# Performance work log

Hardware: AMD Instinct MI355X
Metric: run time of the kernel (lower is better)

Reference implementation:

```python
import jax, jax.numpy as jnp
import numpy as np

B, LQ, LK, D_WORD, D_K, D_V = 8, 2048, 2048, 1024, 128, 128
TEMPERATURE = 11.313708498984761  # sqrt(d_k)
NEG_BIG = -1e9


def setup_inputs() -> dict:
    key = jax.random.key(0)
    ks = jax.random.split(key, 7)
    scale = 1.0 / np.sqrt(D_WORD)
    return {
        "q": jax.random.normal(ks[0], (B, LQ, D_WORD), dtype=jnp.float32),
        "k": jax.random.normal(ks[1], (B, LK, D_WORD), dtype=jnp.float32),
        "v": jax.random.normal(ks[2], (B, LK, D_WORD), dtype=jnp.float32),
        "memory_lengths": jax.random.randint(ks[3], (B,), 1, LK + 1, dtype=jnp.int32),
        "Wq": jax.random.normal(ks[4], (D_WORD, D_K), dtype=jnp.float32) * scale,
        "Wk": jax.random.normal(ks[5], (D_WORD, D_K), dtype=jnp.float32) * scale,
        "Wv": jax.random.normal(ks[6], (D_WORD, D_V), dtype=jnp.float32) * scale,
    }


def reference(q, k, v, memory_lengths, Wq, Wk, Wv):
    # Projections (bias-free Dense layers)
    qs = jnp.einsum("bqw,wd->bqd", q, Wq)   # [B, LQ, D_K]
    ks = jnp.einsum("bkw,wd->bkd", k, Wk)   # [B, LK, D_K]
    vs = jnp.einsum("bkw,wd->bkd", v, Wv)   # [B, LK, D_V]
    # Scaled dot-product scores
    attn = jnp.einsum("bqd,bkd->bqk", qs, ks) / TEMPERATURE  # [B, LQ, LK]
    # Padding mask from memory_lengths (tf.sequence_mask + tile + where)
    mem_mask = jnp.arange(attn.shape[-1])[None, None, :] < memory_lengths[:, None, None]
    attn = jnp.where(mem_mask, attn, NEG_BIG)
    p = jax.nn.softmax(attn, axis=-1)
    return jnp.einsum("bqk,bkd->bqd", p, vs)  # [B, LQ, D_V]
```

## Files before the change

kernel.cpp:

```cpp
#include <hip/hip_runtime.h>

typedef _Float16 half8 __attribute__((ext_vector_type(8)));
typedef float floatx4 __attribute__((ext_vector_type(4)));

#define INV_TEMP 0.08838834764831845f

#define OFF_WT 0
#define OFF_QS (786432)
#define OFF_KS (786432 + 4194304)
#define OFF_VT (786432 + 2 * 4194304)

__global__ __launch_bounds__(256) void wprep_kernel(
    const float* __restrict__ Wq, const float* __restrict__ Wk,
    const float* __restrict__ Wv, _Float16* __restrict__ wt)
{
    int idx = blockIdx.x * 256 + threadIdx.x;
    int m = idx >> 17;
    int rem = idx & 131071;
    int n = rem >> 10;
    int kk = rem & 1023;
    const float* W = (m == 0) ? Wq : (m == 1) ? Wk : Wv;
    float val = W[kk * 128 + n];
    if (m == 0) val *= INV_TEMP;
    wt[idx] = (_Float16)val;
}

__global__ __launch_bounds__(256) void proj_kernel(
    const float* __restrict__ Xq, const float* __restrict__ Xk,
    const float* __restrict__ Xv, const _Float16* __restrict__ wt,
    _Float16* __restrict__ qs, _Float16* __restrict__ ks,
    _Float16* __restrict__ vt)
{
    __shared__ _Float16 smem[64 * 72 + 128 * 72];
    _Float16* As = smem;
    _Float16* Bs = smem + 64 * 72;

    const int t = threadIdx.x;
    const int lane = t & 63;
    const int w = t >> 6;
    const int quad = lane >> 4;
    const int m16 = lane & 15;
    const int yb = blockIdx.y;
    const float* X = (yb == 0) ? Xq : (yb == 1) ? Xk : Xv;
    const _Float16* W = wt + yb * 131072;
    const int m0 = blockIdx.x * 64;

    floatx4 acc[8] = {};

    const int arow = t >> 2, ac4 = t & 3;
    const int bn = t >> 1, bh = t & 1;

    for (int k0 = 0; k0 < 1024; k0 += 64) {
        {
            const float* src = X + (size_t)(m0 + arow) * 1024 + k0 + ac4 * 16;
            float4 f0 = ((const float4*)src)[0];
            float4 f1 = ((const float4*)src)[1];
            float4 f2 = ((const float4*)src)[2];
            float4 f3 = ((const float4*)src)[3];
            _Float16* dst = As + arow * 72 + ac4 * 16;
            half8 h0 = {(_Float16)f0.x, (_Float16)f0.y, (_Float16)f0.z, (_Float16)f0.w,
                        (_Float16)f1.x, (_Float16)f1.y, (_Float16)f1.z, (_Float16)f1.w};
            half8 h1 = {(_Float16)f2.x, (_Float16)f2.y, (_Float16)f2.z, (_Float16)f2.w,
                        (_Float16)f3.x, (_Float16)f3.y, (_Float16)f3.z, (_Float16)f3.w};
            *(half8*)(dst) = h0;
            *(half8*)(dst + 8) = h1;
        }
        {
            const _Float16* src = W + bn * 1024 + k0 + bh * 32;
            _Float16* dst = Bs + bn * 72 + bh * 32;
            #pragma unroll
            for (int i = 0; i < 4; i++)
                *(half8*)(dst + 8 * i) = ((const half8*)src)[i];
        }
        __syncthreads();

        #pragma unroll
        for (int kk = 0; kk < 64; kk += 32) {
            half8 a = *(const half8*)(As + (w * 16 + m16) * 72 + kk + quad * 8);
            #pragma unroll
            for (int nt = 0; nt < 8; nt++) {
                half8 b = *(const half8*)(Bs + (nt * 16 + m16) * 72 + kk + quad * 8);
                acc[nt] = __builtin_amdgcn_mfma_f32_16x16x32_f16(a, b, acc[nt], 0, 0, 0);
            }
        }
        __syncthreads();
    }

    if (yb < 2) {
        _Float16* out = (yb == 0) ? qs : ks;
        #pragma unroll
        for (int nt = 0; nt < 8; nt++) {
            #pragma unroll
            for (int r = 0; r < 4; r++) {
                int row = m0 + w * 16 + quad * 4 + r;
                out[(size_t)row * 128 + nt * 16 + m16] = (_Float16)acc[nt][r];
            }
        }
    } else {
        _Float16* T = smem;
        #pragma unroll
        for (int nt = 0; nt < 8; nt++) {
            #pragma unroll
            for (int r = 0; r < 4; r++)
                T[(w * 16 + quad * 4 + r) * 130 + nt * 16 + m16] = (_Float16)acc[nt][r];
        }
        __syncthreads();
        int dv = t >> 1, hf = t & 1;
        int bb = m0 >> 11;
        int key0 = (m0 & 2047) + hf * 32;
        _Float16* dst = vt + (size_t)(bb * 128 + dv) * 2048 + key0;
        #pragma unroll
        for (int j8 = 0; j8 < 4; j8++) {
            half8 h;
            #pragma unroll
            for (int j = 0; j < 8; j++)
                h[j] = T[(hf * 32 + j8 * 8 + j) * 130 + dv];
            *(half8*)(dst + j8 * 8) = h;
        }
    }
}

__global__ __launch_bounds__(256) void attn_kernel(
    const _Float16* __restrict__ qs, const _Float16* __restrict__ ks,
    const _Float16* __restrict__ vt, const int* __restrict__ mlen,
    float* __restrict__ out)
{
    __shared__ _Float16 kls[64 * 136];
    __shared__ _Float16 vls[128 * 72];
    __shared__ _Float16 pls[4 * 16 * 72];

    const int t = threadIdx.x;
    const int lane = t & 63;
    const int w = t >> 6;
    const int quad = lane >> 4;
    const int m16 = lane & 15;
    const int b = blockIdx.y;
    const int q0 = blockIdx.x * 64;
    const int ml = mlen[b];
    const int nkt = (ml + 63) >> 6;

    half8 aq[4];
    {
        const _Float16* qrow =
            qs + (size_t)(b * 2048 + q0 + w * 16 + m16) * 128 + quad * 8;
        #pragma unroll
        for (int d = 0; d < 4; d++)
            aq[d] = *(const half8*)(qrow + d * 32);
    }

    floatx4 acc[8] = {};
    float m_i[4] = {-3e38f, -3e38f, -3e38f, -3e38f};
    float l_i[4] = {0.f, 0.f, 0.f, 0.f};

    const int skey = t >> 2, sq4 = t & 3;
    const int sdv = t >> 1, shf = t & 1;

    for (int kt = 0; kt < nkt; kt++) {
        const int k0 = kt * 64;
        {
            const _Float16* src = ks + (size_t)(b * 2048 + k0 + skey) * 128 + sq4 * 32;
            _Float16* dst = kls + skey * 136 + sq4 * 32;
            #pragma unroll
            for (int i = 0; i < 4; i++)
                *(half8*)(dst + 8 * i) = ((const half8*)src)[i];
        }
        {
            const _Float16* src = vt + (size_t)(b * 128 + sdv) * 2048 + k0 + shf * 32;
            _Float16* dst = vls + sdv * 72 + shf * 32;
            #pragma unroll
            for (int i = 0; i < 4; i++)
                *(half8*)(dst + 8 * i) = ((const half8*)src)[i];
        }
        __syncthreads();

        floatx4 sacc[4] = {};
        #pragma unroll
        for (int d = 0; d < 4; d++) {
            #pragma unroll
            for (int nt = 0; nt < 4; nt++) {
                half8 bfrag = *(const half8*)(kls + (nt * 16 + m16) * 136 + d * 32 + quad * 8);
                sacc[nt] = __builtin_amdgcn_mfma_f32_16x16x32_f16(aq[d], bfrag, sacc[nt], 0, 0, 0);
            }
        }

        float p[4][4];
        float rowmax[4], rowsum[4];
        #pragma unroll
        for (int r = 0; r < 4; r++) rowmax[r] = -3e38f;
        #pragma unroll
        for (int nt = 0; nt < 4; nt++) {
            int key = k0 + nt * 16 + m16;
            bool valid = key < ml;
            #pragma unroll
            for (int r = 0; r < 4; r++) {
                float s = valid ? sacc[nt][r] : -3e38f;
                p[nt][r] = s;
                rowmax[r] = fmaxf(rowmax[r], s);
            }
        }
        #pragma unroll
        for (int mask = 8; mask >= 1; mask >>= 1) {
            #pragma unroll
            for (int r = 0; r < 4; r++)
                rowmax[r] = fmaxf(rowmax[r], __shfl_xor(rowmax[r], mask, 64));
        }
        #pragma unroll
        for (int r = 0; r < 4; r++) {
            float mnew = fmaxf(m_i[r], rowmax[r]);
            float alpha = __expf(m_i[r] - mnew);
            m_i[r] = mnew;
            l_i[r] *= alpha;
            #pragma unroll
            for (int nt = 0; nt < 8; nt++) acc[nt][r] *= alpha;
            rowsum[r] = 0.f;
            #pragma unroll
            for (int nt = 0; nt < 4; nt++) {
                float e = __expf(p[nt][r] - mnew);
                p[nt][r] = e;
                rowsum[r] += e;
            }
        }
        #pragma unroll
        for (int mask = 8; mask >= 1; mask >>= 1) {
            #pragma unroll
            for (int r = 0; r < 4; r++)
                rowsum[r] += __shfl_xor(rowsum[r], mask, 64);
        }
        #pragma unroll
        for (int r = 0; r < 4; r++) l_i[r] += rowsum[r];

        _Float16* pw = pls + w * 16 * 72;
        #pragma unroll
        for (int nt = 0; nt < 4; nt++) {
            #pragma unroll
            for (int r = 0; r < 4; r++)
                pw[(quad * 4 + r) * 72 + nt * 16 + m16] = (_Float16)p[nt][r];
        }
        __syncthreads();

        #pragma unroll
        for (int kp = 0; kp < 2; kp++) {
            half8 pa = *(const half8*)(pw + m16 * 72 + kp * 32 + quad * 8);
            #pragma unroll
            for (int nt = 0; nt < 8; nt++) {
                half8 bfrag = *(const half8*)(vls + (nt * 16 + m16) * 72 + kp * 32 + quad * 8);
                acc[nt] = __builtin_amdgcn_mfma_f32_16x16x32_f16(pa, bfrag, acc[nt], 0, 0, 0);
            }
        }
        __syncthreads();
    }

    #pragma unroll
    for (int r = 0; r < 4; r++) {
        float inv_l = 1.0f / l_i[r];
        int row = b * 2048 + q0 + w * 16 + quad * 4 + r;
        float* dst = out + (size_t)row * 128;
        #pragma unroll
        for (int nt = 0; nt < 8; nt++)
            dst[nt * 16 + m16] = acc[nt][r] * inv_l;
    }
}

extern "C" void kernel_launch(void* const* d_in, const int* in_sizes, int n_in,
                              void* d_out, int out_size, void* d_ws, size_t ws_size,
                              hipStream_t stream) {
    const float* q   = (const float*)d_in[0];
    const float* k   = (const float*)d_in[1];
    const float* v   = (const float*)d_in[2];
    const int* mlen  = (const int*)d_in[3];
    const float* Wq  = (const float*)d_in[4];
    const float* Wk  = (const float*)d_in[5];
    const float* Wv  = (const float*)d_in[6];
    float* out = (float*)d_out;

    char* ws = (char*)d_ws;
    _Float16* wt = (_Float16*)(ws + OFF_WT);
    _Float16* qs = (_Float16*)(ws + OFF_QS);
    _Float16* kss = (_Float16*)(ws + OFF_KS);
    _Float16* vt = (_Float16*)(ws + OFF_VT);

    hipLaunchKernelGGL(wprep_kernel, dim3(1536), dim3(256), 0, stream, Wq, Wk, Wv, wt);
    hipLaunchKernelGGL(proj_kernel, dim3(256, 3), dim3(256), 0, stream,
                       q, k, v, wt, qs, kss, vt);
    hipLaunchKernelGGL(attn_kernel, dim3(32, 8), dim3(256), 0, stream,
                       qs, kss, vt, mlen, out);
}
```

Measured before the change: 284.6 us.

## Double-buffer projection GEMM with direct-to-LDS weight loads and register A fragments

The projection kernel now stages weight tiles straight into LDS with global_load_lds into a double buffer, using a swizzled k-tile layout that wprep now produces. X rows are loaded directly into registers as MFMA A fragments and prefetched one k-step ahead, so the A-tile LDS staging is gone. The aim is to overlap global loads with MFMA work and cut LDS traffic and bank conflicts. The weight prep kernel is rewritten as a tiled LDS transpose that emits the swizzled layout. The risk is more register pressure and a full waitcnt before each barrier.

```diff
diff --git a/kernel.cpp b/kernel.cpp
--- a/kernel.cpp
+++ b/kernel.cpp
@@ -14,15 +14,39 @@
     const float* __restrict__ Wq, const float* __restrict__ Wk,
     const float* __restrict__ Wv, _Float16* __restrict__ wt)
 {
-    int idx = blockIdx.x * 256 + threadIdx.x;
-    int m = idx >> 17;
-    int rem = idx & 131071;
-    int n = rem >> 10;
-    int kk = rem & 1023;
+    __shared__ _Float16 T[64 * 136];
+    const int t = threadIdx.x;
+    const int kt = blockIdx.x;
+    const int m = blockIdx.y;
     const float* W = (m == 0) ? Wq : (m == 1) ? Wk : Wv;
-    float val = W[kk * 128 + n];
-    if (m == 0) val *= INV_TEMP;
-    wt[idx] = (_Float16)val;
+    const float scale = (m == 0) ? INV_TEMP : 1.0f;
+    const float* src = W + kt * 8192;
+
+    #pragma unroll
+    for (int i = 0; i < 8; i++) {
+        int f = i * 1024 + t * 4;
+        float4 v = *(const float4*)(src + f);
+        int k = f >> 7, n = f & 127;
+        _Float16* d = T + k * 136 + n;
+        d[0] = (_Float16)(v.x * scale);
+        d[1] = (_Float16)(v.y * scale);
+        d[2] = (_Float16)(v.z * scale);
+        d[3] = (_Float16)(v.w * scale);
+    }
+    __syncthreads();
+
+    _Float16* dst = wt + m * 131072 + kt * 8192;
+    #pragma unroll
+    for (int i = 0; i < 4; i++) {
+        int p = i * 256 + t;
+        int n = p >> 3;
+        int c = (p & 7) ^ (n & 7);
+        half8 h;
+        #pragma unroll
+        for (int j = 0; j < 8; j++)
+            h[j] = T[(c * 8 + j) * 136 + n];
+        *(half8*)(dst + p * 8) = h;
+    }
 }
 
 __global__ __launch_bounds__(256) void proj_kernel(
@@ -31,9 +55,7 @@
     _Float16* __restrict__ qs, _Float16* __restrict__ ks,
     _Float16* __restrict__ vt)
 {
-    __shared__ _Float16 smem[64 * 72 + 128 * 72];
-    _Float16* As = smem;
-    _Float16* Bs = smem + 64 * 72;
+    __shared__ _Float16 Bs[2][8192];
 
     const int t = threadIdx.x;
     const int lane = t & 63;
@@ -44,45 +66,65 @@
     const float* X = (yb == 0) ? Xq : (yb == 1) ? Xk : Xv;
     const _Float16* W = wt + yb * 131072;
     const int m0 = blockIdx.x * 64;
+    const int row = m0 + w * 16 + m16;
+    const float* arow = X + (size_t)row * 1024;
 
     floatx4 acc[8] = {};
 
-    const int arow = t >> 2, ac4 = t & 3;
-    const int bn = t >> 1, bh = t & 1;
-
-    for (int k0 = 0; k0 < 1024; k0 += 64) {
-        {
-            const float* src = X + (size_t)(m0 + arow) * 1024 + k0 + ac4 * 16;
-            float4 f0 = ((const float4*)src)[0];
-            float4 f1 = ((const float4*)src)[1];
-            float4 f2 = ((const float4*)src)[2];
-            float4 f3 = ((const float4*)src)[3];
-            _Float16* dst = As + arow * 72 + ac4 * 16;
-            half8 h0 = {(_Float16)f0.x, (_Float16)f0.y, (_Float16)f0.z, (_Float16)f0.w,
-                        (_Float16)f1.x, (_Float16)f1.y, (_Float16)f1.z, (_Float16)f1.w};
-            half8 h1 = {(_Float16)f2.x, (_Float16)f2.y, (_Float16)f2.z, (_Float16)f2.w,
-                        (_Float16)f3.x, (_Float16)f3.y, (_Float16)f3.z, (_Float16)f3.w};
-            *(half8*)(dst) = h0;
-            *(half8*)(dst + 8) = h1;
-        }
-        {
-            const _Float16* src = W + bn * 1024 + k0 + bh * 32;
-            _Float16* dst = Bs + bn * 72 + bh * 32;
-            #pragma unroll
-            for (int i = 0; i < 4; i++)
-                *(half8*)(dst + 8 * i) = ((const half8*)src)[i];
-        }
-        __syncthreads();
-
-        #pragma unroll
-        for (int kk = 0; kk < 64; kk += 32) {
-            half8 a = *(const half8*)(As + (w * 16 + m16) * 72 + kk + quad * 8);
-            #pragma unroll
-            for (int nt = 0; nt < 8; nt++) {
-                half8 b = *(const half8*)(Bs + (nt * 16 + m16) * 72 + kk + quad * 8);
-                acc[nt] = __builtin_amdgcn_mfma_f32_16x16x32_f16(a, b, acc[nt], 0, 0, 0);
-            }
-        }
+    const int sw0 = (quad) ^ (m16 & 7);
+    const int sw1 = (4 + quad) ^ (m16 & 7);
+
+    auto stageB = [&](int buf, int kt) {
+        const _Float16* src = W + kt * 8192;
+        #pragma unroll
+        for (int i = 0; i < 4; i++) {
+            int slotbase = (w * 4 + i) * 64;
+            __builtin_amdgcn_global_load_lds(
+                (const __attribute__((address_space(1))) unsigned int*)(src + (size_t)(slotbase + lane) * 8),
+                (__attribute__((address_space(3))) unsigned int*)(&Bs[buf][(slotbase + lane) * 8]),
+                16, 0, 0);
+        }
+    };
+
+    stageB(0, 0);
+    float4 a0 = *(const float4*)(arow + quad * 8);
+    float4 a1 = *(const float4*)(arow + quad * 8 + 4);
+    float4 a2 = *(const float4*)(arow + 32 + quad * 8);
+    float4 a3 = *(const float4*)(arow + 32 + quad * 8 + 4);
+    __builtin_amdgcn_s_waitcnt(0);
+    __syncthreads();
+
+    for (int kt = 0; kt < 16; kt++) {
+        const int cur = kt & 1;
+        float4 n0, n1, n2, n3;
+        if (kt < 15) {
+            stageB(cur ^ 1, kt + 1);
+            const float* na = arow + (kt + 1) * 64;
+            n0 = *(const float4*)(na + quad * 8);
+            n1 = *(const float4*)(na + quad * 8 + 4);
+            n2 = *(const float4*)(na + 32 + quad * 8);
+            n3 = *(const float4*)(na + 32 + quad * 8 + 4);
+        }
+
+        half8 af0 = {(_Float16)a0.x, (_Float16)a0.y, (_Float16)a0.z, (_Float16)a0.w,
+                     (_Float16)a1.x, (_Float16)a1.y, (_Float16)a1.z, (_Float16)a1.w};
+        half8 af1 = {(_Float16)a2.x, (_Float16)a2.y, (_Float16)a2.z, (_Float16)a2.w,
+                     (_Float16)a3.x, (_Float16)a3.y, (_Float16)a3.z, (_Float16)a3.w};
+
+        const char* bb = (const char*)&Bs[cur][0];
+        #pragma unroll
+        for (int nt = 0; nt < 8; nt++) {
+            half8 bf = *(const half8*)(bb + (nt * 16 + m16) * 128 + sw0 * 16);
+            acc[nt] = __builtin_amdgcn_mfma_f32_16x16x32_f16(af0, bf, acc[nt], 0, 0, 0);
+        }
+        #pragma unroll
+        for (int nt = 0; nt < 8; nt++) {
+            half8 bf = *(const half8*)(bb + (nt * 16 + m16) * 128 + sw1 * 16);
+            acc[nt] = __builtin_amdgcn_mfma_f32_16x16x32_f16(af1, bf, acc[nt], 0, 0, 0);
+        }
+
+        a0 = n0; a1 = n1; a2 = n2; a3 = n3;
+        __builtin_amdgcn_s_waitcnt(0);
         __syncthreads();
     }
 
@@ -92,12 +134,12 @@
         for (int nt = 0; nt < 8; nt++) {
             #pragma unroll
             for (int r = 0; r < 4; r++) {
-                int row = m0 + w * 16 + quad * 4 + r;
-                out[(size_t)row * 128 + nt * 16 + m16] = (_Float16)acc[nt][r];
+                int orow = m0 + w * 16 + quad * 4 + r;
+                out[(size_t)orow * 128 + nt * 16 + m16] = (_Float16)acc[nt][r];
             }
         }
     } else {
-        _Float16* T = smem;
+        _Float16* T = &Bs[0][0];
         #pragma unroll
         for (int nt = 0; nt < 8; nt++) {
             #pragma unroll
@@ -106,9 +148,9 @@
         }
         __syncthreads();
         int dv = t >> 1, hf = t & 1;
-        int bb = m0 >> 11;
+        int bb2 = m0 >> 11;
         int key0 = (m0 & 2047) + hf * 32;
-        _Float16* dst = vt + (size_t)(bb * 128 + dv) * 2048 + key0;
+        _Float16* dst = vt + (size_t)(bb2 * 128 + dv) * 2048 + key0;
         #pragma unroll
         for (int j8 = 0; j8 < 4; j8++) {
             half8 h;
@@ -253,8 +295,8 @@
     #pragma unroll
     for (int r = 0; r < 4; r++) {
         float inv_l = 1.0f / l_i[r];
-        int row = b * 2048 + q0 + w * 16 + quad * 4 + r;
-        float* dst = out + (size_t)row * 128;
+        int orow = b * 2048 + q0 + w * 16 + quad * 4 + r;
+        float* dst = out + (size_t)orow * 128;
         #pragma unroll
         for (int nt = 0; nt < 8; nt++)
             dst[nt * 16 + m16] = acc[nt][r] * inv_l;
@@ -279,7 +321,7 @@
     _Float16* kss = (_Float16*)(ws + OFF_KS);
     _Float16* vt = (_Float16*)(ws + OFF_VT);
 
-    hipLaunchKernelGGL(wprep_kernel, dim3(1536), dim3(256), 0, stream, Wq, Wk, Wv, wt);
+    hipLaunchKernelGGL(wprep_kernel, dim3(16, 3), dim3(256), 0, stream, Wq, Wk, Wv, wt);
     hipLaunchKernelGGL(proj_kernel, dim3(256, 3), dim3(256), 0, stream,
                        q, k, v, wt, qs, kss, vt);
     hipLaunchKernelGGL(attn_kernel, dim3(32, 8), dim3(256), 0, stream,
```

After: 289.0 us. Within noise of the previous version (+1.6%).
